# Performance work log

Measured on AMD Instinct MI355X. Metric: run time of the kernel, lower is better.

## Reference

```python
import jax, jax.numpy as jnp
import numpy as np

D = 512      # model dim
NH = 8       # heads
DH = 64      # dim per head
M = 256      # num landmarks
ITERS = 6    # pinv iterations
EPS = 1e-5   # layernorm eps


def layer_norm(x, g, b):
    mu = x.mean(-1, keepdims=True)
    var = ((x - mu) ** 2).mean(-1, keepdims=True)
    return (x - mu) * jax.lax.rsqrt(var + EPS) * g + b


def moore_penrose_pinv(x, iters=ITERS):
    abs_x = jnp.abs(x)
    col = abs_x.sum(-1)
    row = abs_x.sum(-2)
    z = jnp.swapaxes(x, -1, -2) / (jnp.max(col) * jnp.max(row))
    I = jnp.eye(x.shape[-1], dtype=x.dtype)
    for _ in range(iters):
        xz = x @ z
        z = 0.25 * z @ (13 * I - xz @ (15 * I - xz @ (7 * I - xz)))
    return z


def nystrom_attention(x, w_qkv, w_out, b_out, res_w):
    B, n0, _ = x.shape
    pad = (M - n0 % M) % M
    x = jnp.pad(x, ((0, 0), (pad, 0), (0, 0)))  # pad at front, like lucidrains
    n = n0 + pad
    qkv = x @ w_qkv  # (B, n, 3*D), no bias
    q, k, v = jnp.split(qkv, 3, axis=-1)
    rs = lambda t: t.reshape(B, n, NH, DH).transpose(0, 2, 1, 3)  # (B,H,n,d)
    q = rs(q) * (DH ** -0.5)
    k = rs(k)
    v = rs(v)
    l = n // M
    q_l = q.reshape(B, NH, M, l, DH).mean(3)  # (B,H,M,d) landmark means
    k_l = k.reshape(B, NH, M, l, DH).mean(3)
    s1 = jnp.einsum('bhnd,bhmd->bhnm', q, k_l)
    s2 = jnp.einsum('bhmd,bhld->bhml', q_l, k_l)
    s3 = jnp.einsum('bhmd,bhnd->bhmn', q_l, k)
    a1 = jax.nn.softmax(s1, -1)
    a2 = jax.nn.softmax(s2, -1)
    a3 = jax.nn.softmax(s3, -1)
    out = a1 @ (moore_penrose_pinv(a2) @ (a3 @ v))  # (B,H,n,d)
    # depthwise residual conv over sequence: Conv2d(heads, heads, (33,1), groups=heads)
    res = jax.lax.conv_general_dilated(v, res_w, (1, 1), 'SAME',
                                       feature_group_count=NH,
                                       dimension_numbers=('NCHW', 'OIHW', 'NCHW'))
    out = out + res
    out = out.transpose(0, 2, 1, 3).reshape(B, n, NH * DH) @ w_out + b_out
    return out[:, -n0:]


def dwconv(x, w, b):
    y = jax.lax.conv_general_dilated(x, w, (1, 1), 'SAME',
                                     feature_group_count=x.shape[1],
                                     dimension_numbers=('NCHW', 'OIHW', 'NCHW'))
    return y + b[None, :, None, None]


def ppeg(x, pw7, pb7, pw5, pb5, pw3, pb3, Hh, Ww):
    cls, feat = x[:, :1], x[:, 1:]
    B, _, C = x.shape
    cnn = feat.transpose(0, 2, 1).reshape(B, C, Hh, Ww)
    y = cnn + dwconv(cnn, pw7, pb7) + dwconv(cnn, pw5, pb5) + dwconv(cnn, pw3, pb3)
    y = y.reshape(B, C, Hh * Ww).transpose(0, 2, 1)
    return jnp.concatenate([cls, y], axis=1)


def _forward(x, w_fc1, b_fc1, cls_token, ln1_g, ln1_b, qkv1_w, out1_w, out1_b, res1_w,
             ln2_g, ln2_b, qkv2_w, out2_w, out2_b, res2_w,
             pw7, pb7, pw5, pb5, pw3, pb3, lnf_g, lnf_b, w_fc2, b_fc2):
    h = jax.nn.relu(x @ w_fc1 + b_fc1)  # (B, N, 512)
    Hn = h.shape[1]
    s = int(np.ceil(np.sqrt(Hn)))  # static grid side
    add = s * s - Hn
    h = jnp.concatenate([h, h[:, :add]], axis=1)
    B = h.shape[0]
    cls = jnp.broadcast_to(cls_token, (B, 1, D))
    h = jnp.concatenate([cls, h], axis=1)
    h = h + nystrom_attention(layer_norm(h, ln1_g, ln1_b), qkv1_w, out1_w, out1_b, res1_w)
    h = ppeg(h, pw7, pb7, pw5, pb5, pw3, pb3, s, s)
    h = h + nystrom_attention(layer_norm(h, ln2_g, ln2_b), qkv2_w, out2_w, out2_b, res2_w)
    h = layer_norm(h, lnf_g, lnf_b)[:, 0]
    return h @ w_fc2 + b_fc2


def setup_inputs() -> dict:
    key = jax.random.key(0)
    ks = jax.random.split(key, 16)
    g = lambda k, shp, s=0.02: jax.random.normal(k, shp, dtype=jnp.float32) * s
    z = lambda n: jnp.zeros((n,), jnp.float32)
    o = lambda n: jnp.ones((n,), jnp.float32)
    B, N, DIN, NC = 2, 10000, 1024, 2
    return {
        'x': jax.random.normal(ks[0], (B, N, DIN), dtype=jnp.float32),
        'w_fc1': g(ks[1], (DIN, D)), 'b_fc1': z(D),
        'cls_token': g(ks[2], (1, 1, D), 1.0),
        'ln1_g': o(D), 'ln1_b': z(D),
        'qkv1_w': g(ks[3], (D, 3 * D)),
        'out1_w': g(ks[4], (D, D)), 'out1_b': z(D),
        'res1_w': g(ks[5], (NH, 1, 33, 1)),
        'ln2_g': o(D), 'ln2_b': z(D),
        'qkv2_w': g(ks[6], (D, 3 * D)),
        'out2_w': g(ks[7], (D, D)), 'out2_b': z(D),
        'res2_w': g(ks[8], (NH, 1, 33, 1)),
        'pw7': g(ks[9], (D, 1, 7, 7)), 'pb7': z(D),
        'pw5': g(ks[10], (D, 1, 5, 5)), 'pb5': z(D),
        'pw3': g(ks[11], (D, 1, 3, 3)), 'pb3': z(D),
        'lnf_g': o(D), 'lnf_b': z(D),
        'w_fc2': g(ks[12], (D, NC)), 'b_fc2': z(NC),
    }


def reference(x, w_fc1, b_fc1, cls_token, ln1_g, ln1_b, qkv1_w, out1_w, out1_b, res1_w,
              ln2_g, ln2_b, qkv2_w, out2_w, out2_b, res2_w,
              pw7, pb7, pw5, pb5, pw3, pb3, lnf_g, lnf_b, w_fc2, b_fc2):
    logits = _forward(x, w_fc1, b_fc1, cls_token, ln1_g, ln1_b, qkv1_w, out1_w, out1_b, res1_w,
                      ln2_g, ln2_b, qkv2_w, out2_w, out2_b, res2_w,
                      pw7, pb7, pw5, pb5, pw3, pb3, lnf_g, lnf_b, w_fc2, b_fc2)
    Y_prob = jax.nn.softmax(logits, -1)
    Y_hat = jnp.argmax(logits, -1)
    return logits, Y_prob, Y_hat
```

## Files before the change

### kernel.cpp

```cpp
#include <hip/hip_runtime.h>
#include <math.h>

#define FLAG_RELU 1
#define FLAG_BIAS 2
#define FLAG_ACC  4
#define FLAG_ATOMIC 8

static constexpr int BB   = 2;
static constexpr int N0   = 10000;
static constexpr int DIN  = 1024;
static constexpr int D    = 512;
static constexpr int NH   = 8;
static constexpr int DH   = 64;
static constexpr int MM   = 256;
static constexpr int SEQ  = 10240;
static constexpr int PADR = 239;
static constexpr int NTOK = 10001;
static constexpr int LL   = 40;
static constexpr float EPS_ = 1e-5f;

typedef short short8v __attribute__((ext_vector_type(8)));
typedef float f32x4 __attribute__((ext_vector_type(4)));

__device__ __forceinline__ void atomicMaxPosF(float* addr, float v) {
    atomicMax((unsigned int*)addr, __float_as_uint(v));
}
__device__ __forceinline__ ushort f2bf(float f) {
    unsigned u = __float_as_uint(f);
    return (ushort)((u + 0x7FFFu + ((u >> 16) & 1u)) >> 16);
}
__device__ __forceinline__ float bf2f(ushort h) {
    return __uint_as_float(((unsigned)h) << 16);
}
__device__ __forceinline__ unsigned cvt_pk_bf16(float s0, float s1) {
    unsigned r;
    asm("v_cvt_pk_bf16_f32 %0, %1, %2" : "=v"(r) : "v"(s0), "v"(s1));
    return r;
}
struct bfs4 { unsigned h01, h23, l01, l23; };
__device__ __forceinline__ bfs4 split4pk(float4 f) {
    bfs4 o;
    o.h01 = cvt_pk_bf16(f.x, f.y);
    o.h23 = cvt_pk_bf16(f.z, f.w);
    float hx = __uint_as_float(o.h01 << 16);
    float hy = __uint_as_float(o.h01 & 0xFFFF0000u);
    float hz = __uint_as_float(o.h23 << 16);
    float hw = __uint_as_float(o.h23 & 0xFFFF0000u);
    o.l01 = cvt_pk_bf16(f.x - hx, f.y - hy);
    o.l23 = cvt_pk_bf16(f.z - hz, f.w - hw);
    return o;
}
__device__ __forceinline__ void split8r(const float* p, short8v& h, short8v& l) {
    float4 f0 = *(const float4*)p, f1 = *(const float4*)(p + 4);
    bfs4 a = split4pk(f0), b = split4pk(f1);
    uint4 hu = make_uint4(a.h01, a.h23, b.h01, b.h23);
    uint4 lu = make_uint4(a.l01, a.l23, b.l01, b.l23);
    h = *(short8v*)&hu; l = *(short8v*)&lu;
}

__global__ __launch_bounds__(256)
void mgemm128(const float* __restrict__ A, int lda, long long sAz,
              const ushort* __restrict__ BtH, const ushort* __restrict__ BtL, int ldbt,
              float* __restrict__ C, int ldc, long long sCz, const float* __restrict__ bias,
              int M, int N, int K, int flags, int qcols, float qscale)
{
    __shared__ ushort AsH[4*128*8], AsL[4*128*8], BsH[4*128*8], BsL[4*128*8];
    A += (size_t)blockIdx.z * sAz;
    C += (size_t)blockIdx.z * sCz;
    int t = threadIdx.x;
    int m0 = blockIdx.y * 128, n0 = blockIdx.x * 128;
    int w = t >> 6, lane = t & 63, q = lane >> 4, r = lane & 15;
// ... 37 lines not shown
        if (k0 + 32 < K) {
            pa0 = pa1 = pa2 = pa3 = make_float4(0,0,0,0);
            if (gm < M) {
                const float* ap = A + (size_t)gm * lda + k0 + 32 + scg;
                pa0 = *(const float4*)(ap);   pa1 = *(const float4*)(ap+4);
                pa2 = *(const float4*)(ap+8); pa3 = *(const float4*)(ap+12);
            }
            size_t gb = (size_t)(n0 + srow) * ldbt + k0 + 32 + scg;
            pb0 = *(const uint4*)(BtH + gb); pb1 = *(const uint4*)(BtH + gb + 8);
            pb2 = *(const uint4*)(BtL + gb); pb3 = *(const uint4*)(BtL + gb + 8);
        }
        short8v ah[4], al[4];
        #pragma unroll
        for (int mi = 0; mi < 4; mi++) {
            int row = wm*64 + mi*16 + r;
            ah[mi] = *(const short8v*)&AsH[q*1024 + row*8];
            al[mi] = *(const short8v*)&AsL[q*1024 + row*8];
        }
        #pragma unroll
        for (int ni = 0; ni < 4; ni++) {
            int col = wn*64 + ni*16 + r;
            short8v bh = *(const short8v*)&BsH[q*1024 + col*8];
            short8v bl = *(const short8v*)&BsL[q*1024 + col*8];
            #pragma unroll
            for (int mi = 0; mi < 4; mi++) {
                acc[mi][ni] = __builtin_amdgcn_mfma_f32_16x16x32_bf16(ah[mi], bh, acc[mi][ni], 0,0,0);
                acc[mi][ni] = __builtin_amdgcn_mfma_f32_16x16x32_bf16(ah[mi], bl, acc[mi][ni], 0,0,0);
                acc[mi][ni] = __builtin_amdgcn_mfma_f32_16x16x32_bf16(al[mi], bh, acc[mi][ni], 0,0,0);
            }
        }
        __syncthreads();
    }
    #pragma unroll
    for (int mi = 0; mi < 4; mi++)
        #pragma unroll
        for (int ni = 0; ni < 4; ni++) {
            int gcol = n0 + wn*64 + ni*16 + r;
            float qs = (gcol < qcols) ? qscale : 1.f;
            float bv = (flags & FLAG_BIAS) ? bias[gcol] : 0.f;
            #pragma unroll
            for (int rg = 0; rg < 4; rg++) {
                int grow = m0 + wm*64 + mi*16 + q*4 + rg;
                if (grow >= M) continue;
                float v = acc[mi][ni][rg] * qs + bv;
                if (flags & FLAG_RELU) v = fmaxf(v, 0.f);
                float* cp = C + (size_t)grow * ldc + gcol;
                if (flags & FLAG_ACC) v += *cp;
                *cp = v;
            }
        }
}

__global__ __launch_bounds__(256)
void mbgemm64(const float* __restrict__ Abase, long long sAb, long long sAh, long long sAz, int lda,
              const ushort* __restrict__ BtH, const ushort* __restrict__ BtL,
              const float* __restrict__ Bnt, long long sBb, long long sBh, int ldb,
              float* __restrict__ Cbase, long long sCb, long long sCh, long long sCz, int ldc,
              ushort* __restrict__ eTH, ushort* __restrict__ eTL, long long sT, int ldct,
              const float* __restrict__ rowM, const float* __restrict__ rowI,
              int M, int N, int K, int nchunk,
              float dg, float bsc, float osc, int slab0, int flags)
{
    __shared__ ushort AsH[4*64*8], AsL[4*64*8], BsH[4*64*8], BsL[4*64*8];
    int zi = blockIdx.z / nchunk, ch = blockIdx.z % nchunk;
    int g = slab0 + zi, b = g >> 3, h = g & 7;
    const float* A = Abase + (size_t)b*sAb + (size_t)h*sAh + (size_t)zi*sAz;
    float* C = Cbase ? (Cbase + (size_t)b*sCb + (size_t)h*sCh + (size_t)zi*sCz) : nullptr;
    int kpc = K / nchunk;
    int kb = ch * kpc, ke = kb + kpc;
    int t = threadIdx.x;
    int m0 = blockIdx.y * 64, n0 = blockIdx.x * 64;
    int w = t >> 6, lane = t & 63, q = lane >> 4, r = lane & 15;
    int wm = w >> 1, wn = w & 1;
    f32x4 acc[2][2];
    #pragma unroll
    for (int i = 0; i < 2; i++)
        #pragma unroll
        for (int j = 0; j < 2; j++) acc[i][j] = (f32x4){0.f,0.f,0.f,0.f};

    int srow = t >> 2, scg = (t & 3) * 8;
    int qg = t & 3;
    float rmv = 0.f, riv = 1.f;
    bool doexp = (rowM != nullptr);
    if (doexp) {
        rmv = rowM[(size_t)zi * MM + m0 + srow];
        riv = rowI[(size_t)zi * MM + m0 + srow];
    }
    const float* Abp = Bnt ? (Bnt + (size_t)b*sBb + (size_t)h*sBh) : nullptr;
    float4 pa0, pa1;
    float4 pf0, pf1;
    uint4  pu0, pu1;
    {
        const float* ap = A + (size_t)(m0 + srow) * lda + kb + scg;
        pa0 = *(const float4*)ap; pa1 = *(const float4*)(ap+4);
        if (Bnt) {
            const float* bp = Abp + (size_t)(n0 + srow) * ldb + kb + scg;
            pf0 = *(const float4*)bp; pf1 = *(const float4*)(bp+4);
        } else {
            size_t gb = (size_t)b*sBb + (size_t)h*sBh + (size_t)(n0 + srow) * ldb + kb + scg;
            pu0 = *(const uint4*)(BtH + gb); pu1 = *(const uint4*)(BtL + gb);
        }
    }
    for (int k0 = kb; k0 < ke; k0 += 32) {
        {
            float4 qa0 = pa0, qa1 = pa1;
            if (doexp) {
                qa0.x = __expf(qa0.x - rmv) * riv; qa0.y = __expf(qa0.y - rmv) * riv;
                qa0.z = __expf(qa0.z - rmv) * riv; qa0.w = __expf(qa0.w - rmv) * riv;
                qa1.x = __expf(qa1.x - rmv) * riv; qa1.y = __expf(qa1.y - rmv) * riv;
                qa1.z = __expf(qa1.z - rmv) * riv; qa1.w = __expf(qa1.w - rmv) * riv;
            }
            bfs4 sa0 = split4pk(qa0), sa1 = split4pk(qa1);
            *(uint4*)&AsH[qg*512 + srow*8] = make_uint4(sa0.h01, sa0.h23, sa1.h01, sa1.h23);
            *(uint4*)&AsL[qg*512 + srow*8] = make_uint4(sa0.l01, sa0.l23, sa1.l01, sa1.l23);
            if (Bnt) {
                bfs4 sb0 = split4pk(pf0), sb1 = split4pk(pf1);
                *(uint4*)&BsH[qg*512 + srow*8] = make_uint4(sb0.h01, sb0.h23, sb1.h01, sb1.h23);
                *(uint4*)&BsL[qg*512 + srow*8] = make_uint4(sb0.l01, sb0.l23, sb1.l01, sb1.l23);
            } else {
                *(uint4*)&BsH[qg*512 + srow*8] = pu0;
                *(uint4*)&BsL[qg*512 + srow*8] = pu1;
            }
        }
        __syncthreads();
        if (k0 + 32 < ke) {
            const float* ap = A + (size_t)(m0 + srow) * lda + k0 + 32 + scg;
            pa0 = *(const float4*)ap; pa1 = *(const float4*)(ap+4);
            if (Bnt) {
                const float* bp = Abp + (size_t)(n0 + srow) * ldb + k0 + 32 + scg;
                pf0 = *(const float4*)bp; pf1 = *(const float4*)(bp+4);
            } else {
                size_t gb = (size_t)b*sBb + (size_t)h*sBh + (size_t)(n0 + srow) * ldb + k0 + 32 + scg;
                pu0 = *(const uint4*)(BtH + gb); pu1 = *(const uint4*)(BtL + gb);
            }
        }
        short8v ah[2], al[2];
        #pragma unroll
        for (int mi = 0; mi < 2; mi++) {
            int row = wm*32 + mi*16 + r;
            ah[mi] = *(const short8v*)&AsH[q*512 + row*8];
            al[mi] = *(const short8v*)&AsL[q*512 + row*8];
        }
        #pragma unroll
        for (int ni = 0; ni < 2; ni++) {
            int col = wn*32 + ni*16 + r;
            short8v bh = *(const short8v*)&BsH[q*512 + col*8];
            short8v bl = *(const short8v*)&BsL[q*512 + col*8];
            #pragma unroll
            for (int mi = 0; mi < 2; mi++) {
                acc[mi][ni] = __builtin_amdgcn_mfma_f32_16x16x32_bf16(ah[mi], bh, acc[mi][ni], 0,0,0);
                acc[mi][ni] = __builtin_amdgcn_mfma_f32_16x16x32_bf16(ah[mi], bl, acc[mi][ni], 0,0,0);
                acc[mi][ni] = __builtin_amdgcn_mfma_f32_16x16x32_bf16(al[mi], bh, acc[mi][ni], 0,0,0);
            }
        }
        __syncthreads();
    }
    bool dgnz = (dg != 0.f);
    #pragma unroll
    for (int mi = 0; mi < 2; mi++)
        #pragma unroll
        for (int ni = 0; ni < 2; ni++) {
            int gm0 = m0 + wm*32 + mi*16 + q*4;
            int gn  = n0 + wn*32 + ni*16 + r;
            float v[4];
            #pragma unroll
            for (int rg = 0; rg < 4; rg++) {
                float u = bsc * acc[mi][ni][rg];
                if (dgnz) u += dg * A[(size_t)(gm0+rg) * lda + gn];
                v[rg] = osc * u;
            }
            if (C) {
                if (flags & FLAG_ATOMIC) {
                    #pragma unroll
                    for (int rg = 0; rg < 4; rg++)
                        atomicAdd(C + (size_t)(gm0+rg) * ldc + gn, v[rg]);
                } else {
                    #pragma unroll
                    for (int rg = 0; rg < 4; rg++)
                        C[(size_t)(gm0+rg) * ldc + gn] = v[rg];
                }
            }
            if (eTH) {
                unsigned h01 = cvt_pk_bf16(v[0], v[1]);
                unsigned h23 = cvt_pk_bf16(v[2], v[3]);
                float h0 = __uint_as_float(h01 << 16);
                float h1 = __uint_as_float(h01 & 0xFFFF0000u);
                float h2 = __uint_as_float(h23 << 16);
                float h3 = __uint_as_float(h23 & 0xFFFF0000u);
                unsigned l01 = cvt_pk_bf16(v[0] - h0, v[1] - h1);
                unsigned l23 = cvt_pk_bf16(v[2] - h2, v[3] - h3);
                size_t to = (size_t)g * sT + (size_t)gn * ldct + gm0;
                *(uint2*)(eTH + to) = make_uint2(h01, h23);
                *(uint2*)(eTL + to) = make_uint2(l01, l23);
            }
        }
}

__global__ __launch_bounds__(256)
void mbgemm32(const float* __restrict__ Abase, long long sAz, int lda,
              const ushort* __restrict__ BtH, const ushort* __restrict__ BtL,
              long long sB, int ldb,
              float* __restrict__ Cbase, long long sC, int ldc,
              ushort* __restrict__ eTH, ushort* __restrict__ eTL, long long sT, int ldct,
              int K, float dg, float bsc, float osc)
{
    __shared__ ushort AsH[4*32*8], AsL[4*32*8], BsH[4*32*8], BsL[4*32*8];
    int g = blockIdx.z;
    const float* A = Abase + (size_t)g * sAz;
    float* C = Cbase ? (Cbase + (size_t)g * sC) : nullptr;
    int t = threadIdx.x;
    int m0 = blockIdx.y * 32, n0 = blockIdx.x * 32;
    int w = t >> 6, lane = t & 63, q = lane >> 4, r = lane & 15;
    int wm = w >> 1, wn = w & 1;
    f32x4 acc = (f32x4){0.f,0.f,0.f,0.f};

    int srow = t >> 3, scg = (t & 7) * 4;
    int qg = scg >> 3, qo = scg & 4;
    float4 pa;
    uint2 pbh, pbl;
    {
        pa = *(const float4*)(A + (size_t)(m0 + srow) * lda + scg);
        size_t gb = (size_t)g*sB + (size_t)(n0 + srow) * ldb + scg;
        pbh = *(const uint2*)(BtH + gb); pbl = *(const uint2*)(BtL + gb);
    }
    for (int k0 = 0; k0 < K; k0 += 32) {
        {
            bfs4 s = split4pk(pa);
            *(uint2*)&AsH[qg*256 + srow*8 + qo] = make_uint2(s.h01, s.h23);
            *(uint2*)&AsL[qg*256 + srow*8 + qo] = make_uint2(s.l01, s.l23);
            *(uint2*)&BsH[qg*256 + srow*8 + qo] = pbh;
            *(uint2*)&BsL[qg*256 + srow*8 + qo] = pbl;
        }
        __syncthreads();
        if (k0 + 32 < K) {
            pa = *(const float4*)(A + (size_t)(m0 + srow) * lda + k0 + 32 + scg);
            size_t gb = (size_t)g*sB + (size_t)(n0 + srow) * ldb + k0 + 32 + scg;
            pbh = *(const uint2*)(BtH + gb); pbl = *(const uint2*)(BtL + gb);
        }
        short8v ah = *(const short8v*)&AsH[q*256 + (wm*16 + r)*8];
        short8v al = *(const short8v*)&AsL[q*256 + (wm*16 + r)*8];
        short8v bh = *(const short8v*)&BsH[q*256 + (wn*16 + r)*8];
        short8v bl = *(const short8v*)&BsL[q*256 + (wn*16 + r)*8];
        acc = __builtin_amdgcn_mfma_f32_16x16x32_bf16(ah, bh, acc, 0,0,0);
        acc = __builtin_amdgcn_mfma_f32_16x16x32_bf16(ah, bl, acc, 0,0,0);
        acc = __builtin_amdgcn_mfma_f32_16x16x32_bf16(al, bh, acc, 0,0,0);
        __syncthreads();
    }
    bool dgnz = (dg != 0.f);
    int gm0 = m0 + wm*16 + q*4;
    int gn  = n0 + wn*16 + r;
    float v[4];
    #pragma unroll
    for (int rg = 0; rg < 4; rg++) {
        float u = bsc * acc[rg];
        if (dgnz) u += dg * A[(size_t)(gm0+rg) * lda + gn];
        v[rg] = osc * u;
    }
    if (C) {
        #pragma unroll
        for (int rg = 0; rg < 4; rg++)
            C[(size_t)(gm0+rg) * ldc + gn] = v[rg];
    }
    if (eTH) {
        unsigned h01 = cvt_pk_bf16(v[0], v[1]);
        unsigned h23 = cvt_pk_bf16(v[2], v[3]);
        float h0 = __uint_as_float(h01 << 16);
        float h1 = __uint_as_float(h01 & 0xFFFF0000u);
        float h2 = __uint_as_float(h23 << 16);
        float h3 = __uint_as_float(h23 & 0xFFFF0000u);
        unsigned l01 = cvt_pk_bf16(v[0] - h0, v[1] - h1);
        unsigned l23 = cvt_pk_bf16(v[2] - h2, v[3] - h3);
        size_t to = (size_t)g * sT + (size_t)gn * ldct + gm0;
        *(uint2*)(eTH + to) = make_uint2(h01, h23);
        *(uint2*)(eTL + to) = make_uint2(l01, l23);
    }
}

__global__ __launch_bounds__(256)
void a1_fused(const float* __restrict__ qkv,
              const ushort* __restrict__ klH, const ushort* __restrict__ klL,
              const ushort* __restrict__ wbH, const ushort* __restrict__ wbL,
              float* __restrict__ attn)
{
    constexpr int LP = 264;
    __shared__ ushort PcH[32*LP], PcL[32*LP];
    __shared__ float redm[4][32];
    __shared__ float reds[4][32];
    int g = blockIdx.y, b = g >> 3, h = g & 7;
    int tok0 = blockIdx.x * 32;
    int t = threadIdx.x;
    int w = t >> 6, lane = t & 63, q = lane >> 4, r = lane & 15;

    f32x4 acc[2][4];
    #pragma unroll
    for (int i = 0; i < 2; i++)
        #pragma unroll
        for (int j = 0; j < 4; j++) acc[i][j] = (f32x4){0.f,0.f,0.f,0.f};
    #pragma unroll
    for (int k0 = 0; k0 < 64; k0 += 32) {
        short8v ah[2], al[2];
        #pragma unroll
        for (int mi = 0; mi < 2; mi++) {
            const float* ap = qkv + ((size_t)b*SEQ + tok0 + mi*16 + r) * 1536
                            + h*DH + k0 + q*8;
            split8r(ap, ah[mi], al[mi]);
        }
        #pragma unroll
        for (int ni = 0; ni < 4; ni++) {
            size_t kb = ((size_t)g*MM + w*64 + ni*16 + r) * DH + k0 + q*8;
            short8v bh = *(const short8v*)(klH + kb);
            short8v bl = *(const short8v*)(klL + kb);
            #pragma unroll
            for (int mi = 0; mi < 2; mi++) {
                acc[mi][ni] = __builtin_amdgcn_mfma_f32_16x16x32_bf16(ah[mi], bh, acc[mi][ni], 0,0,0);
                acc[mi][ni] = __builtin_amdgcn_mfma_f32_16x16x32_bf16(ah[mi], bl, acc[mi][ni], 0,0,0);
                acc[mi][ni] = __builtin_amdgcn_mfma_f32_16x16x32_bf16(al[mi], bh, acc[mi][ni], 0,0,0);
            }
        }
    }
    #pragma unroll
    for (int mi = 0; mi < 2; mi++)
        #pragma unroll
        for (int rg = 0; rg < 4; rg++) {
            float m = fmaxf(fmaxf(acc[mi][0][rg], acc[mi][1][rg]),
                            fmaxf(acc[mi][2][rg], acc[mi][3][rg]));
            for (int o = 8; o > 0; o >>= 1) m = fmaxf(m, __shfl_xor(m, o));
            if (r == 0) redm[w][mi*16 + q*4 + rg] = m;
        }
// ... 156 lines not shown
                float* __restrict__ a2)
{
    int blk = blockIdx.x;
    int m = blk & 255, slab = blk >> 8;
    int j = threadIdx.x;
    __shared__ float q[64];
    __shared__ float red[256];
    if (j < 64) q[j] = ql[((size_t)slab * MM + m) * DH + j];
    __syncthreads();
    const float* kt = klt + (size_t)slab * DH * MM;
    float s = 0.f;
    #pragma unroll 8
    for (int kk = 0; kk < 64; kk++) s = fmaf(q[kk], kt[kk*MM + j], s);
    red[j] = s; __syncthreads();
    for (int o = 128; o > 0; o >>= 1) { if (j < o) red[j] = fmaxf(red[j], red[j+o]); __syncthreads(); }
    float mx = red[0]; __syncthreads();
    float e = __expf(s - mx);
    red[j] = e; __syncthreads();
    for (int o = 128; o > 0; o >>= 1) { if (j < o) red[j] += red[j+o]; __syncthreads(); }
    a2[((size_t)slab * MM + m) * MM + j] = e / red[0];
}

__global__ void zero_scr(float* s) { if (threadIdx.x < 2) s[threadIdx.x] = 0.f; }

__global__ __launch_bounds__(256)
void a2_alpha(const float* __restrict__ a2, float* __restrict__ scr)
{
    int slab = blockIdx.x, t = threadIdx.x;
    const float* A = a2 + (size_t)slab * MM * MM;
    float cs = 0.f, rs = 0.f;
    for (int rr = 0; rr < MM; rr++) cs += fabsf(A[(size_t)rr * MM + t]);
    for (int cc = 0; cc < MM; cc++) rs += fabsf(A[(size_t)t * MM + cc]);
    __shared__ float red[256];
    red[t] = rs; __syncthreads();
    for (int o = 128; o > 0; o >>= 1) { if (t < o) red[t] = fmaxf(red[t], red[t+o]); __syncthreads(); }
    float mrs = red[0]; __syncthreads();
    red[t] = cs; __syncthreads();
    for (int o = 128; o > 0; o >>= 1) { if (t < o) red[t] = fmaxf(red[t], red[t+o]); __syncthreads(); }
    float mcs = red[0];
    if (t == 0) { atomicMaxPosF(scr + 0, mrs); atomicMaxPosF(scr + 1, mcs); }
}

__global__ __launch_bounds__(256)
void z_init(const float* __restrict__ a2, const float* __restrict__ scr,
            float* __restrict__ z, ushort* __restrict__ zTh, ushort* __restrict__ zTl)
{
    size_t idx = (size_t)blockIdx.x * 256 + threadIdx.x;
    int slab = (int)(idx >> 16), rr = (int)((idx >> 8) & 255), cc = (int)(idx & 255);
    float inv = 1.0f / (scr[0] * scr[1]);
    z[idx] = a2[((size_t)slab << 16) + (size_t)cc * MM + rr] * inv;
    float tv = a2[idx] * inv;
    ushort th = f2bf(tv);
    zTh[idx] = th; zTl[idx] = f2bf(tv - bf2f(th));
}

__global__ __launch_bounds__(256)
void s3_maxsum(const float* __restrict__ s3, float* __restrict__ rowM,
               float* __restrict__ rowI)
{
    const float* row = s3 + (size_t)blockIdx.x * SEQ;
    int t = threadIdx.x;
    float4 v[10];
    #pragma unroll
    for (int i = 0; i < 10; i++) v[i] = *(const float4*)(row + 4*(i*256 + t));
    float mx = -3.4e38f;
    #pragma unroll
    for (int i = 0; i < 10; i++)
        mx = fmaxf(mx, fmaxf(fmaxf(v[i].x, v[i].y), fmaxf(v[i].z, v[i].w)));
    __shared__ float red[4];
    for (int o = 32; o > 0; o >>= 1) mx = fmaxf(mx, __shfl_xor(mx, o));
    if ((t & 63) == 0) red[t >> 6] = mx;
    __syncthreads();
    mx = fmaxf(fmaxf(red[0], red[1]), fmaxf(red[2], red[3]));
    float sum = 0.f;
    #pragma unroll
    for (int i = 0; i < 10; i++) {
        sum += __expf(v[i].x - mx) + __expf(v[i].y - mx)
             + __expf(v[i].z - mx) + __expf(v[i].w - mx);
    }
    __shared__ float red2[4];
    for (int o = 32; o > 0; o >>= 1) sum += __shfl_xor(sum, o);
    if ((t & 63) == 0) red2[t >> 6] = sum;
    __syncthreads();
    if (t == 0) {
        rowM[blockIdx.x] = mx;
        rowI[blockIdx.x] = 1.0f / (red2[0] + red2[1] + red2[2] + red2[3]);
    }
}

__global__ __launch_bounds__(512)
void res_add(const float* __restrict__ qkv, const float* __restrict__ rw,
             float* __restrict__ attn)
{
    int blk = blockIdx.x;
    int b = blk / (SEQ/16), i0 = (blk % (SEQ/16)) * 16;
    int c = threadIdx.x, h = c >> 6;
    __shared__ float w[NH*33];
    if (c < NH*33) w[c] = rw[c];
    __syncthreads();
    float acc[16];
    float* ab = attn + ((size_t)b * SEQ + i0) * D + c;
    #pragma unroll
    for (int rr = 0; rr < 16; rr++) acc[rr] = ab[(size_t)rr * D];
    const float* vb = qkv + (size_t)b * SEQ * 1536 + 2*D + c;
    const float* wh = w + h * 33;
    #pragma unroll 4
    for (int jj = 0; jj < 48; jj++) {
        int j = i0 + jj - 16;
        float val = ((unsigned)j < (unsigned)SEQ) ? vb[(size_t)j * 1536] : 0.f;
        #pragma unroll
        for (int rr = 0; rr < 16; rr++) {
            int ky = jj - rr;
            if (ky >= 0 && ky < 33) acc[rr] = fmaf(val, wh[ky], acc[rr]);
        }
    }
    #pragma unroll
    for (int rr = 0; rr < 16; rr++) ab[(size_t)rr * D] = acc[rr];
}

__global__ __launch_bounds__(256)
void t_fw(const float* __restrict__ H, float* __restrict__ P)
{
    __shared__ float tile[32][33];
    int p0 = blockIdx.x * 32, c0 = blockIdx.y * 32, b = blockIdx.z;
    int tx = threadIdx.x & 31, ty = threadIdx.x >> 5;
    #pragma unroll
    for (int k = 0; k < 4; k++) {
        int pos = p0 + ty + k*8;
        tile[ty + k*8][tx] = (pos < 10000)
            ? H[((size_t)b * NTOK + 1 + pos) * D + c0 + tx] : 0.f;
    }
    __syncthreads();
    #pragma unroll
    for (int k = 0; k < 4; k++) {
        int c = c0 + ty + k*8, pos = p0 + tx;
        if (pos < 10000)
            P[((size_t)b * D + c) * 10000 + pos] = tile[tx][ty + k*8];
    }
}

// ... 148 lines not shown
    const float* res2_w = (const float*)d_in[15];
    const float* pw7 = (const float*)d_in[16];
    const float* pb7 = (const float*)d_in[17];
    const float* pw5 = (const float*)d_in[18];
    const float* pb5 = (const float*)d_in[19];
    const float* pw3 = (const float*)d_in[20];
    const float* pb3 = (const float*)d_in[21];
    const float* lnf_g = (const float*)d_in[22];
    const float* lnf_b = (const float*)d_in[23];
    const float* w_fc2 = (const float*)d_in[24];
    const float* b_fc2 = (const float*)d_in[25];

    float* ws = (float*)d_ws;
    size_t off = 0;
    auto alloc = [&](size_t n) { float* p = ws + off; off += (n + 63) & ~(size_t)63; return p; };
    float* H    = alloc((size_t)BB * NTOK * D);
    float* LN   = alloc((size_t)BB * SEQ * D);
    float* QKV  = alloc((size_t)BB * SEQ * 3 * D);
    float* QL   = alloc((size_t)BB * NH * MM * DH);
    float* KLT  = alloc((size_t)BB * NH * DH * MM);
    float* A2   = alloc((size_t)BB * NH * MM * MM);
    float* ZA   = alloc((size_t)BB * NH * MM * MM);
    float* ZB   = alloc((size_t)BB * NH * MM * MM);
    float* XZ   = alloc((size_t)BB * NH * MM * MM);
    float* A3V  = alloc((size_t)BB * NH * MM * DH);
    float* WB   = alloc((size_t)BB * NH * MM * DH);
    float* S3   = alloc((size_t)8 * MM * SEQ);
    float* SCR  = alloc(64);
    float* ROWM = alloc((size_t)8 * MM);
    float* ROWI = alloc((size_t)8 * MM);
    auto ualloc = [&](size_t n) { ushort* p = (ushort*)(ws + off); off += ((n + 127) / 2) & ~(size_t)63; return p; };
    ushort* WTfcH = ualloc((size_t)512 * 1024);
    ushort* WTfcL = ualloc((size_t)512 * 1024);
    ushort* WTqH  = ualloc((size_t)1536 * 512);
    ushort* WTqL  = ualloc((size_t)1536 * 512);
    ushort* WToH  = ualloc((size_t)512 * 512);
    ushort* WToL  = ualloc((size_t)512 * 512);
    ushort* klBH  = ualloc((size_t)16 * MM * DH);
    ushort* klBL  = ualloc((size_t)16 * MM * DH);
    float*  ATTN = LN;
    ushort* VTH  = (ushort*)LN;
    ushort* VTL  = VTH + (size_t)16 * DH * SEQ;
    ushort* A3VTH = (ushort*)ZB;
    ushort* A3VTL = A3VTH + (size_t)16 * DH * MM;
    ushort* WBTH  = A3VTL + (size_t)16 * DH * MM;
    ushort* WBTL  = WBTH  + (size_t)16 * DH * MM;
    ushort* PT   = (ushort*)S3;
    const size_t PS_ = (size_t)16 * 65536;
    ushort* zTAH = PT;            ushort* zTAL = PT + PS_;
    ushort* zTBH = PT + 2*PS_;    ushort* zTBL = PT + 3*PS_;
    ushort* XZTH = PT + 4*PS_;    ushort* XZTL = PT + 5*PS_;
    ushort* T1TH = PT + 6*PS_;    ushort* T1TL = PT + 7*PS_;
    ushort* T2TH = PT + 8*PS_;    ushort* T2TL = PT + 9*PS_;
    (void)ws_size; (void)in_sizes; (void)n_in; (void)out_size;

    convsplitT<<<dim3(32,16,1), 256, 0, stream>>>(w_fc1, WTfcH, WTfcL, 1024, 512, 512, 0,0,0, 1024, 0);
    mgemm128<<<dim3(4, 79, BB), 256, 0, stream>>>(x, DIN, (long long)N0*DIN,
        WTfcH, WTfcL, 1024, H + D, D, (long long)NTOK*D, b_fc1,
        N0, D, DIN, FLAG_BIAS|FLAG_RELU, 0, 1.f);
    fill_cls<<<BB, D, 0, stream>>>(cls, H);

    auto attention = [&](const float* lg, const float* lb,
                         const float* qw, const float* ow,
                         const float* ob, const float* rw)
    {
        convsplitT<<<dim3(16,48,1), 256, 0, stream>>>(qw, WTqH, WTqL, 512, 1536, 1536, 0,0,0, 512, 0);
        convsplitT<<<dim3(16,16,1), 256, 0, stream>>>(ow, WToH, WToL, 512, 512, 512, 0,0,0, 512, 0);
        ln_pad<<<BB*SEQ, 256, 0, stream>>>(H, lg, lb, LN);
        mgemm128<<<dim3(12, 160, 1), 256, 0, stream>>>(LN, D, 0, WTqH, WTqL, D,
            QKV, 3*D, 0, nullptr, BB*SEQ, 3*D, D, 0, D, 0.125f);
        convsplitT<<<dim3(320, 2, 16), 256, 0, stream>>>(QKV + 2*D, VTH, VTL,
            SEQ, DH, 1536, (long long)SEQ*1536, 64, 0, SEQ, (long long)DH*SEQ);
        landmarks<<<BB*MM, 512, 0, stream>>>(QKV, QL, KLT, klBH, klBL);
        s2_softmax<<<BB*NH*MM, 256, 0, stream>>>(QL, KLT, A2);
        zero_scr<<<1, 64, 0, stream>>>(SCR);
        a2_alpha<<<BB*NH, 256, 0, stream>>>(A2, SCR);
        z_init<<<BB*NH*MM*MM/256, 256, 0, stream>>>(A2, SCR, ZA, zTAH, zTAL);
        float* z = ZA; float* zn = ZB;
        ushort *zTcH = zTAH, *zTcL = zTAL, *zTnH = zTBH, *zTnL = zTBL;
        for (int it = 0; it < 6; it++) {
            dim3 g(8, 8, 16);
            mbgemm32<<<g,256,0,stream>>>(A2, 65536LL, MM,
                zTcH, zTcL, 65536LL, MM,
                XZ, 65536LL, MM, XZTH, XZTL, 65536LL, MM,
                MM, 0.f, 1.f, 1.f);
            mbgemm32<<<g,256,0,stream>>>(XZ, 65536LL, MM,
                XZTH, XZTL, 65536LL, MM,
                nullptr, 0, MM, T1TH, T1TL, 65536LL, MM,
                MM, 7.f, -1.f, 1.f);
            mbgemm32<<<g,256,0,stream>>>(XZ, 65536LL, MM,
                T1TH, T1TL, 65536LL, MM,
                nullptr, 0, MM, T2TH, T2TL, 65536LL, MM,
                MM, 15.f, -1.f, 1.f);
            mbgemm32<<<g,256,0,stream>>>(z, 65536LL, MM,
                T2TH, T2TL, 65536LL, MM,
                zn, 65536LL, MM, zTnH, zTnL, 65536LL, MM,
                MM, 13.f, -1.f, 0.25f);
            float* ts = z; z = zn; zn = ts;
            ushort* uh = zTcH; zTcH = zTnH; zTnH = uh;
            ushort* ul = zTcL; zTcL = zTnL; zTnL = ul;
        }
        for (int grp = 0; grp < 2; grp++) {
            int slab0 = grp * 8;
            mbgemm64<<<dim3(160, 4, 8), 256, 0, stream>>>(QL, 8LL*16384, 16384LL, 0, DH,
                nullptr, nullptr, QKV + D, (long long)SEQ*1536, 64LL, 1536,
                S3, 0,0,(long long)MM*SEQ, SEQ, nullptr, nullptr, 0, 0,
                nullptr, nullptr,
                MM, SEQ, DH, 1, 0.f, 1.f, 1.f, slab0, 0);
            s3_maxsum<<<8*MM, 256, 0, stream>>>(S3, ROWM, ROWI);
            hipMemsetAsync(A3V + (size_t)slab0 * MM * DH, 0,
                           (size_t)8 * MM * DH * sizeof(float), stream);
            mbgemm64<<<dim3(1, 4, 8*16), 256, 0, stream>>>(S3, 0,0,(long long)MM*SEQ, SEQ,
                VTH, VTL, nullptr, 8LL*DH*SEQ, (long long)DH*SEQ, SEQ,
                A3V, 8LL*16384, 16384LL, 0, DH, nullptr, nullptr, 0, 0,
                ROWM, ROWI,
                MM, DH, SEQ, 16, 0.f, 1.f, 1.f, slab0, FLAG_ATOMIC);
        }
        convsplitT<<<dim3(8, 2, 16), 256, 0, stream>>>(A3V, A3VTH, A3VTL,
            MM, DH, DH, 0, 0, 16384LL, MM, 16384LL);
        mbgemm32<<<dim3(2, 8, 16), 256, 0, stream>>>(z, 65536LL, MM,
            A3VTH, A3VTL, 16384LL, MM,
            WB, 16384LL, DH, WBTH, WBTL, 16384LL, MM,
            MM, 0.f, 1.f, 1.f);
        a1_fused<<<dim3(SEQ/32, 16), 256, 0, stream>>>(QKV, klBH, klBL, WBTH, WBTL, ATTN);
        res_add<<<BB*SEQ/16, 512, 0, stream>>>(QKV, rw, ATTN);
        mgemm128<<<dim3(4, 79, BB), 256, 0, stream>>>(ATTN + (size_t)PADR*D, D, (long long)SEQ*D,
            WToH, WToL, D, H, D, (long long)NTOK*D, ob,
            NTOK, D, D, FLAG_BIAS|FLAG_ACC, 0, 1.f);
    };

    attention(ln1_g, ln1_b, qkv1_w, out1_w, out1_b, res1_w);

    {
        float* Pp = S3;
        float* Qp = S3 + (size_t)BB * D * 10000;
        dim3 tg((10000 + 31)/32, D/32, BB);
        t_fw<<<tg, 256, 0, stream>>>(H, Pp);
        ppeg_conv<<<BB*D, 256, 0, stream>>>(Pp, pw7, pb7, pw5, pb5, pw3, pb3, Qp);
        t_bw<<<tg, 256, 0, stream>>>(Qp, H);
    }

    attention(ln2_g, ln2_b, qkv2_w, out2_w, out2_b, res2_w);

    final_head<<<BB, 512, 0, stream>>>(H, lnf_g, lnf_b, w_fc2, b_fc2, (float*)d_out);
}
```

Before: 2.210 ms.

## Fuse landmark-to-token softmax attention into flash-style split-K kernel with combine pass

Replaces the S3 score GEMM, the row max/sum pass, the memset and the atomic-add A3·V GEMM, plus the transpose-split, with a single flash-attention-style kernel. It computes q_l·k scores per 64-token tile, keeps an online softmax per landmark row, and accumulates P·V across 16 sequence chunks. A small combine kernel then merges the chunk partials and writes the bf16 hi/lo transposed result directly. This drops the full S3 materialisation (256×10240 per head) and its repeated global reads, at the cost of more syncs per tile and K/V loaded straight from global memory without LDS staging.

```diff
diff --git a/kernel.cpp b/kernel.cpp
--- a/kernel.cpp
+++ b/kernel.cpp
@@ -4,7 +4,6 @@
 #define FLAG_RELU 1
 #define FLAG_BIAS 2
 #define FLAG_ACC  4
-#define FLAG_ATOMIC 8
 
 static constexpr int BB   = 2;
 static constexpr int N0   = 10000;
@@ -17,6 +16,7 @@
 static constexpr int PADR = 239;
 static constexpr int NTOK = 10001;
 static constexpr int LL   = 40;
+static constexpr int NCH  = 16;
 static constexpr float EPS_ = 1e-5f;
 
 typedef short short8v __attribute__((ext_vector_type(8)));
@@ -160,151 +160,6 @@
 }
 
 __global__ __launch_bounds__(256)
-void mbgemm64(const float* __restrict__ Abase, long long sAb, long long sAh, long long sAz, int lda,
-              const ushort* __restrict__ BtH, const ushort* __restrict__ BtL,
-              const float* __restrict__ Bnt, long long sBb, long long sBh, int ldb,
-              float* __restrict__ Cbase, long long sCb, long long sCh, long long sCz, int ldc,
-              ushort* __restrict__ eTH, ushort* __restrict__ eTL, long long sT, int ldct,
-              const float* __restrict__ rowM, const float* __restrict__ rowI,
-              int M, int N, int K, int nchunk,
-              float dg, float bsc, float osc, int slab0, int flags)
-{
-    __shared__ ushort AsH[4*64*8], AsL[4*64*8], BsH[4*64*8], BsL[4*64*8];
-    int zi = blockIdx.z / nchunk, ch = blockIdx.z % nchunk;
-    int g = slab0 + zi, b = g >> 3, h = g & 7;
-    const float* A = Abase + (size_t)b*sAb + (size_t)h*sAh + (size_t)zi*sAz;
-    float* C = Cbase ? (Cbase + (size_t)b*sCb + (size_t)h*sCh + (size_t)zi*sCz) : nullptr;
-    int kpc = K / nchunk;
-    int kb = ch * kpc, ke = kb + kpc;
-    int t = threadIdx.x;
-    int m0 = blockIdx.y * 64, n0 = blockIdx.x * 64;
-    int w = t >> 6, lane = t & 63, q = lane >> 4, r = lane & 15;
-    int wm = w >> 1, wn = w & 1;
-    f32x4 acc[2][2];
-    #pragma unroll
-    for (int i = 0; i < 2; i++)
-        #pragma unroll
-        for (int j = 0; j < 2; j++) acc[i][j] = (f32x4){0.f,0.f,0.f,0.f};
-
-    int srow = t >> 2, scg = (t & 3) * 8;
-    int qg = t & 3;
-    float rmv = 0.f, riv = 1.f;
-    bool doexp = (rowM != nullptr);
-    if (doexp) {
-        rmv = rowM[(size_t)zi * MM + m0 + srow];
-        riv = rowI[(size_t)zi * MM + m0 + srow];
-    }
-    const float* Abp = Bnt ? (Bnt + (size_t)b*sBb + (size_t)h*sBh) : nullptr;
-    float4 pa0, pa1;
-    float4 pf0, pf1;
-    uint4  pu0, pu1;
-    {
-        const float* ap = A + (size_t)(m0 + srow) * lda + kb + scg;
-        pa0 = *(const float4*)ap; pa1 = *(const float4*)(ap+4);
-        if (Bnt) {
-            const float* bp = Abp + (size_t)(n0 + srow) * ldb + kb + scg;
-            pf0 = *(const float4*)bp; pf1 = *(const float4*)(bp+4);
-        } else {
-            size_t gb = (size_t)b*sBb + (size_t)h*sBh + (size_t)(n0 + srow) * ldb + kb + scg;
-            pu0 = *(const uint4*)(BtH + gb); pu1 = *(const uint4*)(BtL + gb);
-        }
-    }
-    for (int k0 = kb; k0 < ke; k0 += 32) {
-        {
-            float4 qa0 = pa0, qa1 = pa1;
-            if (doexp) {
-                qa0.x = __expf(qa0.x - rmv) * riv; qa0.y = __expf(qa0.y - rmv) * riv;
-                qa0.z = __expf(qa0.z - rmv) * riv; qa0.w = __expf(qa0.w - rmv) * riv;
-                qa1.x = __expf(qa1.x - rmv) * riv; qa1.y = __expf(qa1.y - rmv) * riv;
-                qa1.z = __expf(qa1.z - rmv) * riv; qa1.w = __expf(qa1.w - rmv) * riv;
-            }
-            bfs4 sa0 = split4pk(qa0), sa1 = split4pk(qa1);
-            *(uint4*)&AsH[qg*512 + srow*8] = make_uint4(sa0.h01, sa0.h23, sa1.h01, sa1.h23);
-            *(uint4*)&AsL[qg*512 + srow*8] = make_uint4(sa0.l01, sa0.l23, sa1.l01, sa1.l23);
-            if (Bnt) {
-                bfs4 sb0 = split4pk(pf0), sb1 = split4pk(pf1);
-                *(uint4*)&BsH[qg*512 + srow*8] = make_uint4(sb0.h01, sb0.h23, sb1.h01, sb1.h23);
-                *(uint4*)&BsL[qg*512 + srow*8] = make_uint4(sb0.l01, sb0.l23, sb1.l01, sb1.l23);
-            } else {
-                *(uint4*)&BsH[qg*512 + srow*8] = pu0;
-                *(uint4*)&BsL[qg*512 + srow*8] = pu1;
-            }
-        }
-        __syncthreads();
-        if (k0 + 32 < ke) {
-            const float* ap = A + (size_t)(m0 + srow) * lda + k0 + 32 + scg;
-            pa0 = *(const float4*)ap; pa1 = *(const float4*)(ap+4);
-            if (Bnt) {
-                const float* bp = Abp + (size_t)(n0 + srow) * ldb + k0 + 32 + scg;
-                pf0 = *(const float4*)bp; pf1 = *(const float4*)(bp+4);
-            } else {
-                size_t gb = (size_t)b*sBb + (size_t)h*sBh + (size_t)(n0 + srow) * ldb + k0 + 32 + scg;
-                pu0 = *(const uint4*)(BtH + gb); pu1 = *(const uint4*)(BtL + gb);
-            }
-        }
-        short8v ah[2], al[2];
-        #pragma unroll
-        for (int mi = 0; mi < 2; mi++) {
-            int row = wm*32 + mi*16 + r;
-            ah[mi] = *(const short8v*)&AsH[q*512 + row*8];
-            al[mi] = *(const short8v*)&AsL[q*512 + row*8];
-        }
-        #pragma unroll
-        for (int ni = 0; ni < 2; ni++) {
-            int col = wn*32 + ni*16 + r;
-            short8v bh = *(const short8v*)&BsH[q*512 + col*8];
-            short8v bl = *(const short8v*)&BsL[q*512 + col*8];
-            #pragma unroll
-            for (int mi = 0; mi < 2; mi++) {
-                acc[mi][ni] = __builtin_amdgcn_mfma_f32_16x16x32_bf16(ah[mi], bh, acc[mi][ni], 0,0,0);
-                acc[mi][ni] = __builtin_amdgcn_mfma_f32_16x16x32_bf16(ah[mi], bl, acc[mi][ni], 0,0,0);
-                acc[mi][ni] = __builtin_amdgcn_mfma_f32_16x16x32_bf16(al[mi], bh, acc[mi][ni], 0,0,0);
-            }
-        }
-        __syncthreads();
-    }
-    bool dgnz = (dg != 0.f);
-    #pragma unroll
-    for (int mi = 0; mi < 2; mi++)
-        #pragma unroll
-        for (int ni = 0; ni < 2; ni++) {
-            int gm0 = m0 + wm*32 + mi*16 + q*4;
-            int gn  = n0 + wn*32 + ni*16 + r;
-            float v[4];
-            #pragma unroll
-            for (int rg = 0; rg < 4; rg++) {
-                float u = bsc * acc[mi][ni][rg];
-                if (dgnz) u += dg * A[(size_t)(gm0+rg) * lda + gn];
-                v[rg] = osc * u;
-            }
-            if (C) {
-                if (flags & FLAG_ATOMIC) {
-                    #pragma unroll
-                    for (int rg = 0; rg < 4; rg++)
-                        atomicAdd(C + (size_t)(gm0+rg) * ldc + gn, v[rg]);
-                } else {
-                    #pragma unroll
-                    for (int rg = 0; rg < 4; rg++)
-                        C[(size_t)(gm0+rg) * ldc + gn] = v[rg];
-                }
-            }
-            if (eTH) {
-                unsigned h01 = cvt_pk_bf16(v[0], v[1]);
-                unsigned h23 = cvt_pk_bf16(v[2], v[3]);
-                float h0 = __uint_as_float(h01 << 16);
-                float h1 = __uint_as_float(h01 & 0xFFFF0000u);
-                float h2 = __uint_as_float(h23 << 16);
-                float h3 = __uint_as_float(h23 & 0xFFFF0000u);
-                unsigned l01 = cvt_pk_bf16(v[0] - h0, v[1] - h1);
-                unsigned l23 = cvt_pk_bf16(v[2] - h2, v[3] - h3);
-                size_t to = (size_t)g * sT + (size_t)gn * ldct + gm0;
-                *(uint2*)(eTH + to) = make_uint2(h01, h23);
-                *(uint2*)(eTL + to) = make_uint2(l01, l23);
-            }
-        }
-}
-
-__global__ __launch_bounds__(256)
 void mbgemm32(const float* __restrict__ Abase, long long sAz, int lda,
               const ushort* __restrict__ BtH, const ushort* __restrict__ BtL,
               long long sB, int ldb,
@@ -382,6 +237,171 @@
         *(uint2*)(eTH + to) = make_uint2(h01, h23);
         *(uint2*)(eTL + to) = make_uint2(l01, l23);
     }
+}
+
+__global__ __launch_bounds__(256)
+void a3v_flash(const float* __restrict__ ql, const float* __restrict__ qkv,
+               const ushort* __restrict__ vtH, const ushort* __restrict__ vtL,
+               float* __restrict__ PO, float* __restrict__ PM, float* __restrict__ PL)
+{
+    constexpr int LP  = 72;
+    constexpr int CHT = SEQ / NCH;
+    __shared__ ushort PcH[64*LP], PcL[64*LP];
+    __shared__ float redm[2][64], reds[2][64];
+    __shared__ float mrun[64], lrun[64];
+    int ch = blockIdx.x, my = blockIdx.y, g = blockIdx.z;
+    int b = g >> 3, h = g & 7;
+    int t = threadIdx.x;
+    int w = t >> 6, lane = t & 63, q = lane >> 4, r = lane & 15;
+    int wm = w >> 1, wn = w & 1;
+
+    if (t < 64) { mrun[t] = -3.4e38f; lrun[t] = 0.f; }
+
+    short8v qh[2][2], qlo[2][2];
+    #pragma unroll
+    for (int mi = 0; mi < 2; mi++)
+        #pragma unroll
+        for (int k0 = 0; k0 < 2; k0++) {
+            const float* ap = ql + ((size_t)g*MM + my*64 + wm*32 + mi*16 + r) * DH
+                            + k0*32 + q*8;
+            split8r(ap, qh[mi][k0], qlo[mi][k0]);
+        }
+    const float* Kb = qkv + (size_t)b*SEQ*1536 + D + h*DH;
+    const ushort* vH = vtH + (size_t)g*DH*SEQ;
+    const ushort* vL = vtL + (size_t)g*DH*SEQ;
+    f32x4 oacc[2][2];
+    #pragma unroll
+    for (int i = 0; i < 2; i++)
+        #pragma unroll
+        for (int j = 0; j < 2; j++) oacc[i][j] = (f32x4){0.f,0.f,0.f,0.f};
+    __syncthreads();
+
+    for (int tt = 0; tt < CHT/64; tt++) {
+        int tok0 = ch*CHT + tt*64;
+        f32x4 sacc[2][2];
+        #pragma unroll
+        for (int i = 0; i < 2; i++)
+            #pragma unroll
+            for (int j = 0; j < 2; j++) sacc[i][j] = (f32x4){0.f,0.f,0.f,0.f};
+        #pragma unroll
+        for (int k0 = 0; k0 < 2; k0++)
+            #pragma unroll
+            for (int ni = 0; ni < 2; ni++) {
+                short8v bh, bl;
+                split8r(Kb + (size_t)(tok0 + wn*32 + ni*16 + r)*1536 + k0*32 + q*8, bh, bl);
+                #pragma unroll
+                for (int mi = 0; mi < 2; mi++) {
+                    sacc[mi][ni] = __builtin_amdgcn_mfma_f32_16x16x32_bf16(qh[mi][k0], bh, sacc[mi][ni], 0,0,0);
+                    sacc[mi][ni] = __builtin_amdgcn_mfma_f32_16x16x32_bf16(qh[mi][k0], bl, sacc[mi][ni], 0,0,0);
+                    sacc[mi][ni] = __builtin_amdgcn_mfma_f32_16x16x32_bf16(qlo[mi][k0], bh, sacc[mi][ni], 0,0,0);
+                }
+            }
+        #pragma unroll
+        for (int mi = 0; mi < 2; mi++)
+            #pragma unroll
+            for (int rg = 0; rg < 4; rg++) {
+                float m = fmaxf(sacc[mi][0][rg], sacc[mi][1][rg]);
+                for (int o = 8; o > 0; o >>= 1) m = fmaxf(m, __shfl_xor(m, o));
+                if (r == 0) redm[wn][wm*32 + mi*16 + q*4 + rg] = m;
+            }
+        __syncthreads();
+        float scv[2][4], mnv[2][4];
+        #pragma unroll
+        for (int mi = 0; mi < 2; mi++)
+            #pragma unroll
+            for (int rg = 0; rg < 4; rg++) {
+                int row = wm*32 + mi*16 + q*4 + rg;
+                float tm = fmaxf(redm[0][row], redm[1][row]);
+                float mo = mrun[row];
+                float mn = fmaxf(mo, tm);
+                float sc = __expf(mo - mn);
+                scv[mi][rg] = sc; mnv[mi][rg] = mn;
+                float e0 = __expf(sacc[mi][0][rg] - mn);
+                float e1 = __expf(sacc[mi][1][rg] - mn);
+                float s = e0 + e1;
+                unsigned h01 = cvt_pk_bf16(e0, e1);
+                float r0 = __uint_as_float(h01 << 16);
+                float r1 = __uint_as_float(h01 & 0xFFFF0000u);
+                unsigned l01 = cvt_pk_bf16(e0 - r0, e1 - r1);
+                int cb = row*LP + wn*32 + r;
+                PcH[cb     ] = (ushort)h01;
+                PcH[cb + 16] = (ushort)(h01 >> 16);
+                PcL[cb     ] = (ushort)l01;
+                PcL[cb + 16] = (ushort)(l01 >> 16);
+                oacc[mi][0][rg] *= sc;
+                oacc[mi][1][rg] *= sc;
+                for (int o = 8; o > 0; o >>= 1) s += __shfl_xor(s, o);
+                if (r == 0) reds[wn][row] = s;
+            }
+        __syncthreads();
+        if (wn == 0 && r == 0) {
+            #pragma unroll
+            for (int mi = 0; mi < 2; mi++)
+                #pragma unroll
+                for (int rg = 0; rg < 4; rg++) {
+                    int row = wm*32 + mi*16 + q*4 + rg;
+                    lrun[row] = lrun[row]*scv[mi][rg] + reds[0][row] + reds[1][row];
+                    mrun[row] = mnv[mi][rg];
+                }
+        }
+        #pragma unroll
+        for (int k0 = 0; k0 < 2; k0++)
+            #pragma unroll
+            for (int mi = 0; mi < 2; mi++) {
+                int prow = wm*32 + mi*16 + r;
+                short8v ph = *(const short8v*)&PcH[prow*LP + k0*32 + q*8];
+                short8v pl = *(const short8v*)&PcL[prow*LP + k0*32 + q*8];
+                #pragma unroll
+                for (int nd = 0; nd < 2; nd++) {
+                    size_t vo = ((size_t)(wn*32 + nd*16 + r))*SEQ + tok0 + k0*32 + q*8;
+                    short8v vh = *(const short8v*)(vH + vo);
+                    short8v vl = *(const short8v*)(vL + vo);
+                    oacc[mi][nd] = __builtin_amdgcn_mfma_f32_16x16x32_bf16(ph, vh, oacc[mi][nd], 0,0,0);
+                    oacc[mi][nd] = __builtin_amdgcn_mfma_f32_16x16x32_bf16(ph, vl, oacc[mi][nd], 0,0,0);
+                    oacc[mi][nd] = __builtin_amdgcn_mfma_f32_16x16x32_bf16(pl, vh, oacc[mi][nd], 0,0,0);
+                }
+            }
+        __syncthreads();
+    }
+    size_t pbase = ((size_t)g*NCH + ch)*MM + my*64;
+    #pragma unroll
+    for (int mi = 0; mi < 2; mi++)
+        #pragma unroll
+        for (int nd = 0; nd < 2; nd++)
+            #pragma unroll
+            for (int rg = 0; rg < 4; rg++) {
+                int row = wm*32 + mi*16 + q*4 + rg;
+                int col = wn*32 + nd*16 + r;
+                PO[(pbase + row)*64 + col] = oacc[mi][nd][rg];
+            }
+    if (t < 64) {
+        PM[pbase + t] = mrun[t];
+        PL[pbase + t] = lrun[t];
+    }
+}
+
+__global__ __launch_bounds__(256)
+void a3v_comb(const float* __restrict__ PO, const float* __restrict__ PM,
+              const float* __restrict__ PL, ushort* __restrict__ oh, ushort* __restrict__ ol)
+{
+    int w = threadIdx.x >> 6, lane = threadIdx.x & 63;
+    int gid = blockIdx.x * 4 + w;
+    int g = gid >> 8, rowm = gid & 255;
+    size_t base = (size_t)g*NCH*MM + rowm;
+    float m = -3.4e38f;
+    #pragma unroll
+    for (int ch = 0; ch < NCH; ch++) m = fmaxf(m, PM[base + (size_t)ch*MM]);
+    float l = 0.f, o = 0.f;
+    #pragma unroll
+    for (int ch = 0; ch < NCH; ch++) {
+        float f = __expf(PM[base + (size_t)ch*MM] - m);
+        l += PL[base + (size_t)ch*MM] * f;
+        o += PO[(base + (size_t)ch*MM)*64 + lane] * f;
+    }
+    float val = o / l;
+    ushort hv = f2bf(val);
+    size_t oo = (size_t)g*DH*MM + (size_t)lane*MM + rowm;
+    oh[oo] = hv; ol[oo] = f2bf(val - bf2f(hv));
 }
 
 __global__ __launch_bounds__(256)
@@ -644,40 +664,6 @@
     float tv = a2[idx] * inv;
     ushort th = f2bf(tv);
     zTh[idx] = th; zTl[idx] = f2bf(tv - bf2f(th));
-}
-
-__global__ __launch_bounds__(256)
-void s3_maxsum(const float* __restrict__ s3, float* __restrict__ rowM,
-               float* __restrict__ rowI)
-{
-    const float* row = s3 + (size_t)blockIdx.x * SEQ;
-    int t = threadIdx.x;
-    float4 v[10];
-    #pragma unroll
-    for (int i = 0; i < 10; i++) v[i] = *(const float4*)(row + 4*(i*256 + t));
-    float mx = -3.4e38f;
-    #pragma unroll
-    for (int i = 0; i < 10; i++)
-        mx = fmaxf(mx, fmaxf(fmaxf(v[i].x, v[i].y), fmaxf(v[i].z, v[i].w)));
-    __shared__ float red[4];
-    for (int o = 32; o > 0; o >>= 1) mx = fmaxf(mx, __shfl_xor(mx, o));
-    if ((t & 63) == 0) red[t >> 6] = mx;
-    __syncthreads();
-    mx = fmaxf(fmaxf(red[0], red[1]), fmaxf(red[2], red[3]));
-    float sum = 0.f;
-    #pragma unroll
-    for (int i = 0; i < 10; i++) {
-        sum += __expf(v[i].x - mx) + __expf(v[i].y - mx)
-             + __expf(v[i].z - mx) + __expf(v[i].w - mx);
-    }
-    __shared__ float red2[4];
-    for (int o = 32; o > 0; o >>= 1) sum += __shfl_xor(sum, o);
-    if ((t & 63) == 0) red2[t >> 6] = sum;
-    __syncthreads();
-    if (t == 0) {
-        rowM[blockIdx.x] = mx;
-        rowI[blockIdx.x] = 1.0f / (red2[0] + red2[1] + red2[2] + red2[3]);
-    }
 }
 
 __global__ __launch_bounds__(512)
@@ -932,7 +918,11 @@
     ushort* XZTH = PT + 4*PS_;    ushort* XZTL = PT + 5*PS_;
     ushort* T1TH = PT + 6*PS_;    ushort* T1TL = PT + 7*PS_;
     ushort* T2TH = PT + 8*PS_;    ushort* T2TL = PT + 9*PS_;
+    float* PO = S3;
+    float* PM = S3 + (size_t)16 * NCH * MM * 64;
+    float* PL = PM + (size_t)16 * NCH * MM;
     (void)ws_size; (void)in_sizes; (void)n_in; (void)out_size;
+    (void)A3V; (void)ROWM; (void)ROWI;
 
     convsplitT<<<dim3(32,16,1), 256, 0, stream>>>(w_fc1, WTfcH, WTfcL, 1024, 512, 512, 0,0,0, 1024, 0);
     mgemm128<<<dim3(4, 79, BB), 256, 0, stream>>>(x, DIN, (long long)N0*DIN,
@@ -980,24 +970,8 @@
             ushort* uh = zTcH; zTcH = zTnH; zTnH = uh;
             ushort* ul = zTcL; zTcL = zTnL; zTnL = ul;
         }
-        for (int grp = 0; grp < 2; grp++) {
-            int slab0 = grp * 8;
-            mbgemm64<<<dim3(160, 4, 8), 256, 0, stream>>>(QL, 8LL*16384, 16384LL, 0, DH,
-                nullptr, nullptr, QKV + D, (long long)SEQ*1536, 64LL, 1536,
-                S3, 0,0,(long long)MM*SEQ, SEQ, nullptr, nullptr, 0, 0,
-                nullptr, nullptr,
-                MM, SEQ, DH, 1, 0.f, 1.f, 1.f, slab0, 0);
-            s3_maxsum<<<8*MM, 256, 0, stream>>>(S3, ROWM, ROWI);
-            hipMemsetAsync(A3V + (size_t)slab0 * MM * DH, 0,
-                           (size_t)8 * MM * DH * sizeof(float), stream);
-            mbgemm64<<<dim3(1, 4, 8*16), 256, 0, stream>>>(S3, 0,0,(long long)MM*SEQ, SEQ,
-                VTH, VTL, nullptr, 8LL*DH*SEQ, (long long)DH*SEQ, SEQ,
-                A3V, 8LL*16384, 16384LL, 0, DH, nullptr, nullptr, 0, 0,
-                ROWM, ROWI,
-                MM, DH, SEQ, 16, 0.f, 1.f, 1.f, slab0, FLAG_ATOMIC);
-        }
-        convsplitT<<<dim3(8, 2, 16), 256, 0, stream>>>(A3V, A3VTH, A3VTL,
-            MM, DH, DH, 0, 0, 16384LL, MM, 16384LL);
+        a3v_flash<<<dim3(NCH, 4, 16), 256, 0, stream>>>(QL, QKV, VTH, VTL, PO, PM, PL);
+        a3v_comb<<<dim3(16*MM/4), 256, 0, stream>>>(PO, PM, PL, A3VTH, A3VTL);
         mbgemm32<<<dim3(2, 8, 16), 256, 0, stream>>>(z, 65536LL, MM,
             A3VTH, A3VTL, 16384LL, MM,
             WB, 16384LL, DH, WBTH, WBTL, 16384LL, MM,
```

New measurement: 2.164 ms. -2.1%, faster.
